# Performance work log

Hardware: AMD Instinct MI355X
Metric: run time of the kernel (lower is better)

The kernel has to match this reference:

```python
import math
import itertools
import jax, jax.numpy as jnp
import numpy as np

SEQ_LEN = 16
D_IN = 2048
TSS = 3          # temporal_set_size
D_OUT = 1128
PE_SCALE = 0.1
N_SUPPORT = 5
N_QUERIES = 1
LN_EPS = 1e-5


def _pos_enc(seq_len, d_model):
    pos = np.arange(seq_len, dtype=np.float32)[:, None]
    div = np.exp(np.arange(0, d_model, 2, dtype=np.float32) * -(math.log(10000.0) / d_model))
    pe = np.zeros((seq_len, d_model), dtype=np.float32)
    pe[:, 0::2] = np.sin(pos * div) * PE_SCALE
    pe[:, 1::2] = np.cos(pos * div) * PE_SCALE
    return jnp.asarray(pe)


def _tuples(seq_len, k):
    return np.asarray(list(itertools.combinations(range(seq_len), k)), dtype=np.int32)  # [T, k]


def setup_inputs() -> dict:
    key = jax.random.key(0)
    ks = jax.random.split(key, 8)
    return {
        "support_set": jax.random.normal(ks[0], (N_SUPPORT, SEQ_LEN, D_IN), jnp.float32),
        "queries": jax.random.normal(ks[1], (N_QUERIES, SEQ_LEN, D_IN), jnp.float32),
        "support_labels": jnp.arange(N_SUPPORT, dtype=jnp.int64),
        "wk": jax.random.normal(ks[2], (D_OUT, D_IN * TSS), jnp.float32) * 0.02,
        "bk": jax.random.normal(ks[3], (D_OUT,), jnp.float32) * 0.02,
        "wv": jax.random.normal(ks[4], (D_OUT, D_IN * TSS), jnp.float32) * 0.02,
        "bv": jax.random.normal(ks[5], (D_OUT,), jnp.float32) * 0.02,
        "gamma": jnp.ones((D_OUT,), jnp.float32),
        "beta": jnp.zeros((D_OUT,), jnp.float32),
    }


def _layer_norm(x, gamma, beta):
    mu = jnp.mean(x, axis=-1, keepdims=True)
    var = jnp.mean(jnp.square(x - mu), axis=-1, keepdims=True)
    return (x - mu) * jax.lax.rsqrt(var + LN_EPS) * gamma + beta


def reference(support_set, queries, support_labels, wk, bk, wv, bv, gamma, beta):
    tup = _tuples(SEQ_LEN, TSS)                      # [T, 3] static
    T = tup.shape[0]                                 # tuples_len = C(16,3) = 560
    pe = _pos_enc(SEQ_LEN, D_IN)                     # [S, D_IN]

    s = support_set + pe                             # [5, S, D_IN]
    q = queries + pe                                 # [1, S, D_IN]

    # gather frame tuples and flatten: [n, T, 3*D_IN]
    s_t = s[:, tup, :].reshape(N_SUPPORT, T, TSS * D_IN)
    q_t = q[:, tup, :].reshape(N_QUERIES, T, TSS * D_IN)

    s_ks = _layer_norm(s_t @ wk.T + bk, gamma, beta)  # [5, T, D_OUT]
    q_ks = _layer_norm(q_t @ wk.T + bk, gamma, beta)  # [1, T, D_OUT]
    s_vs = s_t @ wv.T + bv                            # [5, T, D_OUT]
    q_vs = q_t @ wv.T + bv                            # [1, T, D_OUT]

    # _extract_class_indices returns the label value itself -> direct row gather
    ck = s_ks[support_labels]                         # [C, T, D_OUT]
    cv = s_vs[support_labels]                         # [C, T, D_OUT]

    scores = jnp.einsum('qtd,csd->cqts', q_ks, ck) / math.sqrt(D_OUT)  # [C, Q, T, T]
    attn = jax.nn.softmax(scores, axis=-1)            # softmax over support tuples
    proto = jnp.einsum('cqts,csd->cqtd', attn, cv)    # [C, Q, T, D_OUT]

    diff = q_vs[None] - proto                         # [C, Q, T, D_OUT]
    dist = -jnp.sum(diff * diff, axis=(-2, -1)) / T   # [C, Q]
    logits = dist.T                                   # [Q, C]
    return logits
```

## Files before the change

kernel.cpp:

```cpp
#include <hip/hip_runtime.h>
#include <hip/hip_bf16.h>

#define SEQ 16
#define DIN 2048
#define TSS 3
#define DOUT 1128
#define DPAD 1152
#define NT 560
#define NTPAD 576
#define NSEQ 6
#define NCOL 6768

typedef __attribute__((ext_vector_type(4))) float f32x4;
typedef __attribute__((ext_vector_type(8))) short bf16x8;

__device__ __forceinline__ float bf2f(unsigned short h) {
    union { unsigned int u; float f; } c; c.u = ((unsigned int)h) << 16; return c.f;
}
__device__ __forceinline__ unsigned short f2bf(float f) {
    union { float f; unsigned int u; } c; c.f = f;
    unsigned int lsb = (c.u >> 16) & 1;
    c.u += 0x7fffu + lsb;
    return (unsigned short)(c.u >> 16);
}
__device__ __forceinline__ float loadf(const void* p, size_t i, int f32m) {
    return f32m ? ((const float*)p)[i] : bf2f(((const unsigned short*)p)[i]);
}
__device__ __forceinline__ void load8(const void* p, int o, int f32m, float* out) {
    if (f32m) {
        f32x4 x0 = *(const f32x4*)((const float*)p + o);
        f32x4 x1 = *(const f32x4*)((const float*)p + o + 4);
#pragma unroll
        for (int j = 0; j < 4; ++j) { out[j] = x0[j]; out[4 + j] = x1[j]; }
    } else {
        bf16x8 h = *(const bf16x8*)((const unsigned short*)p + o);
#pragma unroll
        for (int j = 0; j < 8; ++j) out[j] = bf2f((unsigned short)h[j]);
    }
}
__device__ __forceinline__ int probe_f32(const void* gamma) {
    return (((const unsigned int*)gamma)[0] == 0x3F800000u) ? 1 : 0;
}
__device__ __forceinline__ int probe_i64(const void* labels) {
    return (((const long long*)labels)[1] == 1LL) ? 1 : 0;
}
__device__ __forceinline__ int get_label(const void* p, int c, int is64) {
    long long v = is64 ? ((const long long*)p)[c] : (long long)((const int*)p)[c];
    if (v < 0) v = 0; if (v > 4) v = 4;
    return (int)v;
}


__global__ __launch_bounds__(256) void k_build_x(
        const void* __restrict__ sup, const void* __restrict__ qry,
        const void* __restrict__ gamma,
        unsigned short* __restrict__ XF) {
    int f32m = probe_f32(gamma);
    int c8 = blockIdx.x * 256 + threadIdx.x;
    int idx512 = c8 >> 6;
    int rowgrp = idx512 >> 6, kt = idx512 & 63;
    int sub = c8 & 63;
    int r15 = sub & 15;
    int row = rowgrp * 16 + r15;
    int f = row & 15, n = row >> 4;
    int k = kt * 32 + (sub >> 4) * 8;
    bf16x8 ov;
#pragma unroll
    for (int j = 0; j < 8; ++j) {
        int d = k + j;
        float v = (n < 5) ? loadf(sup, (size_t)row * DIN + d, f32m)
                          : loadf(qry, (size_t)f * DIN + d, f32m);
        int m2 = d & ~1;
        float div = __expf(-(float)m2 * (9.210340371976184f / 2048.0f));
        float ang = (float)f * div;
        float pe = ((d & 1) ? __cosf(ang) : __sinf(ang)) * 0.1f;
        ov[j] = (short)f2bf(v + pe);
    }
    *(bf16x8*)(XF + (size_t)c8 * 8) = ov;
}

__global__ __launch_bounds__(512) void k_proj(
        const unsigned short* __restrict__ XF,
        const void* __restrict__ wk, const void* __restrict__ wv,
        const void* __restrict__ gamma,
        unsigned short* __restrict__ Pb) {
    int f32m = probe_f32(gamma);
    int cg = blockIdx.x;
    int tid = threadIdx.x;
    int w = tid >> 6, lane = tid & 63;
    int c16 = lane & 15, quad = lane >> 4;
    int col = cg * 16 + c16;
    int which = col / 3384; int rem = col - which * 3384;
    int seg = rem / DOUT;   int o = rem - seg * DOUT;
    const void* src = which ? wv : wk;
    size_t sbase = (size_t)o * (TSS * DIN) + (size_t)seg * DIN + (size_t)quad * 8;
    const unsigned short* aF = XF + lane * 8;

    f32x4 acc[6];
#pragma unroll
    for (int m = 0; m < 6; ++m) acc[m] = (f32x4){0.f, 0.f, 0.f, 0.f};

    int ktb = w * 8;
    if (f32m) {
        const float* s32 = (const float*)src + sbase;
#pragma unroll 2
        for (int kt = ktb; kt < ktb + 8; ++kt) {
            f32x4 w0 = *(const f32x4*)(s32 + (size_t)kt * 32);
            f32x4 w1 = *(const f32x4*)(s32 + (size_t)kt * 32 + 4);
            bf16x8 b;
#pragma unroll
            for (int j = 0; j < 4; ++j) {
                b[j]     = (short)f2bf(w0[j]);
                b[4 + j] = (short)f2bf(w1[j]);
            }
#pragma unroll
            for (int m = 0; m < 6; ++m) {
                bf16x8 a = *(const bf16x8*)(aF + ((size_t)(m * 64 + kt) << 9));
                acc[m] = __builtin_amdgcn_mfma_f32_16x16x32_bf16(a, b, acc[m], 0, 0, 0);
            }
        }
    } else {
        const unsigned short* s16 = (const unsigned short*)src + sbase;
#pragma unroll 2
        for (int kt = ktb; kt < ktb + 8; ++kt) {
            bf16x8 b = *(const bf16x8*)(s16 + (size_t)kt * 32);
#pragma unroll
            for (int m = 0; m < 6; ++m) {
                bf16x8 a = *(const bf16x8*)(aF + ((size_t)(m * 64 + kt) << 9));
                acc[m] = __builtin_amdgcn_mfma_f32_16x16x32_bf16(a, b, acc[m], 0, 0, 0);
            }
        }
    }

    __shared__ float red[8 * 6 * 64 * 4];
#pragma unroll
    for (int m = 0; m < 6; ++m)
#pragma unroll
        for (int r = 0; r < 4; ++r)
            red[(((w) * 6 + m) * 64 + lane) * 4 + r] = acc[m][r];
    __syncthreads();
    if (w < 6) {
        int m = w;
#pragma unroll
        for (int r = 0; r < 4; ++r) {
            float s = 0.f;
#pragma unroll
            for (int k = 0; k < 8; ++k)
                s += red[((k * 6 + m) * 64 + lane) * 4 + r];
            int row = m * 16 + quad * 4 + r;
            Pb[(size_t)row * NCOL + col] = f2bf(s);
        }
    }
}

__global__ __launch_bounds__(192) void k_combine_ln(
        const unsigned short* __restrict__ Pb,
        const void* __restrict__ bk, const void* __restrict__ bv,
        const void* __restrict__ gamma, const void* __restrict__ beta,
        unsigned short* __restrict__ ksF, unsigned short* __restrict__ vs) {
    int n = blockIdx.x / NT, t = blockIdx.x % NT;
    int f32m = probe_f32(gamma);
    int idx = t, fi, fj, fk;
    for (fi = 0;; ++fi) { int c2 = (15 - fi) * (14 - fi) / 2; if (idx < c2) break; idx -= c2; }
    for (fj = fi + 1;; ++fj) { int c1 = 15 - fj; if (idx < c1) break; idx -= c1; }
    fk = fj + 1 + idx;
    size_t ri = (size_t)(n * 16 + fi) * NCOL;
    size_t rj = (size_t)(n * 16 + fj) * NCOL;
    size_t rk = (size_t)(n * 16 + fk) * NCOL;

    int c = threadIdx.x;
    int o = c * 8;
    float av[8], bvv[8];
    float s = 0.f, s2 = 0.f;
    if (c < 141) {
        bf16x8 p0 = *(const bf16x8*)(Pb + ri + o);
        bf16x8 p1 = *(const bf16x8*)(Pb + rj + DOUT + o);
        bf16x8 p2 = *(const bf16x8*)(Pb + rk + 2 * DOUT + o);
        bf16x8 p3 = *(const bf16x8*)(Pb + ri + 3 * DOUT + o);
        bf16x8 p4 = *(const bf16x8*)(Pb + rj + 4 * DOUT + o);
        bf16x8 p5 = *(const bf16x8*)(Pb + rk + 5 * DOUT + o);
        float kb[8], vb[8];
        load8(bk, o, f32m, kb);
        load8(bv, o, f32m, vb);
#pragma unroll
        for (int e = 0; e < 8; ++e) {
            float a = bf2f((unsigned short)p0[e]) + bf2f((unsigned short)p1[e])
                    + bf2f((unsigned short)p2[e]) + kb[e];
            float b = bf2f((unsigned short)p3[e]) + bf2f((unsigned short)p4[e])
                    + bf2f((unsigned short)p5[e]) + vb[e];
            av[e] = a; bvv[e] = b;
            s += a; s2 += a * a;
        }
    }
    __shared__ float red[6];
#pragma unroll
    for (int off = 32; off; off >>= 1) { s += __shfl_down(s, off); s2 += __shfl_down(s2, off); }
    int wid = threadIdx.x >> 6;
    if ((threadIdx.x & 63) == 0) { red[wid] = s; red[3 + wid] = s2; }
    __syncthreads();
    s = red[0] + red[1] + red[2];
    s2 = red[3] + red[4] + red[5];
    float mu = s / (float)DOUT;
    float var = s2 / (float)DOUT - mu * mu;
    float rstd = rsqrtf(var + 1e-5f);

    size_t ntbase = ((size_t)(n * 36 + (t >> 4)) * 36) * 512 + (size_t)(t & 15) * 8;
    size_t vbase = ((size_t)n * NT + t) * DPAD;
    if (c < 144) {
        bf16x8 kout = (bf16x8){0, 0, 0, 0, 0, 0, 0, 0};
        bf16x8 vout = (bf16x8){0, 0, 0, 0, 0, 0, 0, 0};
        if (c < 141) {
            float gb[8], be[8];
            load8(gamma, o, f32m, gb);
            load8(beta, o, f32m, be);
#pragma unroll
            for (int e = 0; e < 8; ++e) {
                kout[e] = (short)f2bf((av[e] - mu) * rstd * gb[e] + be[e]);
                vout[e] = (short)f2bf(bvv[e]);
            }
        }
        *(bf16x8*)(ksF + ntbase + ((size_t)(c >> 2) << 9) + ((size_t)(c & 3) << 7)) = kout;
        *(bf16x8*)(vs + vbase + o) = vout;
    }
}

__global__ __launch_bounds__(128) void k_transpose(
        const unsigned short* __restrict__ vs, unsigned short* __restrict__ vsTF) {
    int b = blockIdx.x;
    int tt = b % 18; b /= 18; int ot = b % 36; int n = b / 36;
    int t0 = tt * 32, o0 = ot * 32;
    int tid = threadIdx.x;
    __shared__ unsigned short tile[32][33];
    {
        int tl = tid >> 2, ch = tid & 3;
        int t = t0 + tl;
        bf16x8 v = (bf16x8){0, 0, 0, 0, 0, 0, 0, 0};
        if (t < NT) v = *(const bf16x8*)(vs + ((size_t)n * NT + t) * DPAD + o0 + ch * 8);
#pragma unroll
        for (int j = 0; j < 8; ++j) tile[tl][ch * 8 + j] = (unsigned short)v[j];
    }
    __syncthreads();
    {
        int r = tid >> 2, g = tid & 3;
        union { unsigned short u[8]; bf16x8 v; } pk;
#pragma unroll
        for (int e = 0; e < 8; ++e) pk.u[e] = tile[g * 8 + e][r];
        size_t addr = ((size_t)(n * 72 + ot * 2 + (r >> 4)) * 18 + tt) * 512
                    + (size_t)(g * 16 + (r & 15)) * 8;
        *(bf16x8*)(vsTF + addr) = pk.v;
    }
}

__global__ __launch_bounds__(256) void k_scores(
        const unsigned short* __restrict__ ksF, const void* __restrict__ labels,
        float* __restrict__ scores) {
    int b = blockIdx.x;
    int c = b % 5; int rest = b / 5;
    int tm = rest / 9, tn = rest % 9;
    int tid = threadIdx.x;
    int w = tid >> 6, lane = tid & 63;
    int c16 = lane & 15, quad = lane >> 4;
    int lab = get_label(labels, c, probe_i64(labels));
    const unsigned short* aF[4];
    const unsigned short* bF[4];
#pragma unroll
    for (int i = 0; i < 4; ++i) {
        aF[i] = ksF + (((size_t)(5 * 36 + tm * 4 + i) * 36) << 9) + lane * 8;
        bF[i] = ksF + (((size_t)(lab * 36 + tn * 4 + i) * 36) << 9) + lane * 8;
    }
    f32x4 acc[4][4];
#pragma unroll
    for (int i = 0; i < 4; ++i)
#pragma unroll
        for (int j = 0; j < 4; ++j) acc[i][j] = (f32x4){0.f, 0.f, 0.f, 0.f};

    int ktb = w * 9;
#pragma unroll 2
    for (int kt = ktb; kt < ktb + 9; ++kt) {
        bf16x8 a[4], bv4[4];
#pragma unroll
        for (int i = 0; i < 4; ++i) a[i]   = *(const bf16x8*)(aF[i] + ((size_t)kt << 9));
#pragma unroll
        for (int j = 0; j < 4; ++j) bv4[j] = *(const bf16x8*)(bF[j] + ((size_t)kt << 9));
#pragma unroll
        for (int i = 0; i < 4; ++i)
#pragma unroll
            for (int j = 0; j < 4; ++j)
                acc[i][j] = __builtin_amdgcn_mfma_f32_16x16x32_bf16(a[i], bv4[j], acc[i][j], 0, 0, 0);
    }
    __shared__ float red[16 * 3 * 64 * 4];
#pragma unroll
    for (int i = 0; i < 4; ++i) {
        if (i != w) {
            int slot = (w < i) ? w : w - 1;
#pragma unroll
            for (int j = 0; j < 4; ++j)
#pragma unroll
                for (int r = 0; r < 4; ++r)
                    red[(((i * 4 + j) * 3 + slot) * 64 + lane) * 4 + r] = acc[i][j][r];
        }
    }
    __syncthreads();
    {
        const float scale = 0.029774540f;
        f32x4 own[4];
        if (w == 0)      { own[0]=acc[0][0]; own[1]=acc[0][1]; own[2]=acc[0][2]; own[3]=acc[0][3]; }
        else if (w == 1) { own[0]=acc[1][0]; own[1]=acc[1][1]; own[2]=acc[1][2]; own[3]=acc[1][3]; }
        else if (w == 2) { own[0]=acc[2][0]; own[1]=acc[2][1]; own[2]=acc[2][2]; own[3]=acc[2][3]; }
        else             { own[0]=acc[3][0]; own[1]=acc[3][1]; own[2]=acc[3][2]; own[3]=acc[3][3]; }
#pragma unroll
        for (int j = 0; j < 4; ++j) {
            int t = w * 4 + j;
#pragma unroll
            for (int r = 0; r < 4; ++r) {
                float s = 0.f;
#pragma unroll
                for (int k = 0; k < 4; ++k) {
                    if (k == w) s += own[j][r];
                    else {
                        int slot = k - (k > w ? 1 : 0);
                        s += red[((t * 3 + slot) * 64 + lane) * 4 + r];
                    }
                }
                int tq = tm * 64 + w * 16 + quad * 4 + r;
                int ts = tn * 64 + j * 16 + c16;
                scores[((size_t)c * NTPAD + tq) * NTPAD + ts] = s * scale;
            }
        }
    }
}

__global__ __launch_bounds__(256) void k_softmax(
        const float* __restrict__ scores, unsigned short* __restrict__ attnF) {
    int row = blockIdx.x * 4 + (threadIdx.x >> 6);
    int lane = threadIdx.x & 63;
    int c = row / NTPAD, tq = row % NTPAD;
    unsigned short* dstc = attnF + ((size_t)(c * 36 + (tq >> 4)) * 18) * 512 + (size_t)(tq & 15) * 8;
    if (tq >= NT) {
#pragma unroll
        for (int i = 0; i < 9; ++i) {
            int ts = lane + i * 64;
            dstc[((ts >> 5) << 9) + ((ts >> 3) & 3) * 128 + (ts & 7)] = 0;
        }
        return;
    }
    const float* src = scores + (size_t)row * NTPAD;
    float vals[9];
    float m = -1e30f;
#pragma unroll
    for (int i = 0; i < 9; ++i) {
        int idx = lane + i * 64;
        vals[i] = (idx < NT) ? src[idx] : -1e30f;
        m = fmaxf(m, vals[i]);
    }
#pragma unroll
    for (int off = 32; off; off >>= 1) m = fmaxf(m, __shfl_xor(m, off));
    float s = 0.f;
#pragma unroll
    for (int i = 0; i < 9; ++i) {
        int idx = lane + i * 64;
        vals[i] = (idx < NT) ? __expf(vals[i] - m) : 0.f;
        s += vals[i];
    }
#pragma unroll
    for (int off = 32; off; off >>= 1) s += __shfl_xor(s, off);
    float inv = 1.f / s;
#pragma unroll
    for (int i = 0; i < 9; ++i) {
        int ts = lane + i * 64;
        dstc[((ts >> 5) << 9) + ((ts >> 3) & 3) * 128 + (ts & 7)] =
            (ts < NT) ? f2bf(vals[i] * inv) : 0;
    }
}

__global__ __launch_bounds__(128) void k_proto_dist(
        const unsigned short* __restrict__ attnF, const unsigned short* __restrict__ vs,
        const unsigned short* __restrict__ vsTF,
        const void* __restrict__ labels, float* __restrict__ parts) {
    int b = blockIdx.x;
    int c = b / 162; int rest = b % 162;
    int tm = rest / 18, tn = rest % 18;
    int tid = threadIdx.x;
    int w = tid >> 6, lane = tid & 63;
    int c16 = lane & 15, quad = lane >> 4;
    int lab = get_label(labels, c, probe_i64(labels));
    const unsigned short* aF = attnF + ((size_t)(c * 36 + tm * 4) * 18) * 512 + lane * 8;
    const unsigned short* bF = vsTF + ((size_t)(lab * 72 + tn * 4) * 18) * 512 + lane * 8;
    f32x4 acc[4][4];
#pragma unroll
    for (int i = 0; i < 4; ++i)
#pragma unroll
        for (int j = 0; j < 4; ++j) acc[i][j] = (f32x4){0.f, 0.f, 0.f, 0.f};

    int ktb = w * 9;
#pragma unroll 2
    for (int kt = ktb; kt < ktb + 9; ++kt) {
        bf16x8 a[4], bv4[4];
#pragma unroll
        for (int i = 0; i < 4; ++i) a[i]   = *(const bf16x8*)(aF + ((size_t)(i * 18 + kt) << 9));
#pragma unroll
        for (int j = 0; j < 4; ++j) bv4[j] = *(const bf16x8*)(bF + ((size_t)(j * 18 + kt) << 9));
#pragma unroll
        for (int i = 0; i < 4; ++i)
#pragma unroll
            for (int j = 0; j < 4; ++j)
                acc[i][j] = __builtin_amdgcn_mfma_f32_16x16x32_bf16(a[i], bv4[j], acc[i][j], 0, 0, 0);
    }
    __shared__ float red[16 * 64 * 4];
    if (w == 0) {
#pragma unroll
        for (int i = 2; i < 4; ++i)
#pragma unroll
            for (int j = 0; j < 4; ++j)
#pragma unroll
                for (int r = 0; r < 4; ++r)
                    red[((i * 4 + j) * 64 + lane) * 4 + r] = acc[i][j][r];
    } else {
#pragma unroll
        for (int i = 0; i < 2; ++i)
#pragma unroll
            for (int j = 0; j < 4; ++j)
#pragma unroll
                for (int r = 0; r < 4; ++r)
                    red[((i * 4 + j) * 64 + lane) * 4 + r] = acc[i][j][r];
    }
    __syncthreads();
    {
        const unsigned short* qv = vs + (size_t)5 * NT * DPAD;
        float part = 0.f;
        if (w == 0) {
#pragma unroll
            for (int i = 0; i < 2; ++i)
#pragma unroll
                for (int j = 0; j < 4; ++j)
#pragma unroll
                    for (int r = 0; r < 4; ++r) {
                        float s = acc[i][j][r] + red[((i * 4 + j) * 64 + lane) * 4 + r];
                        int tq = tm * 64 + i * 16 + quad * 4 + r;
                        int o  = tn * 64 + j * 16 + c16;
                        if (tq < NT && o < DOUT) {
                            float d = bf2f(qv[(size_t)tq * DPAD + o]) - s;
                            part += d * d;
                        }
                    }
        } else {
#pragma unroll
            for (int i = 2; i < 4; ++i)
#pragma unroll
                for (int j = 0; j < 4; ++j)
#pragma unroll
                    for (int r = 0; r < 4; ++r) {
                        float s = acc[i][j][r] + red[((i * 4 + j) * 64 + lane) * 4 + r];
                        int tq = tm * 64 + i * 16 + quad * 4 + r;
                        int o  = tn * 64 + j * 16 + c16;
                        if (tq < NT && o < DOUT) {
                            float d = bf2f(qv[(size_t)tq * DPAD + o]) - s;
                            part += d * d;
                        }
                    }
        }
#pragma unroll
        for (int off = 32; off; off >>= 1) part += __shfl_down(part, off);
        if (lane == 0) parts[blockIdx.x * 2 + w] = part;
    }
}

__global__ __launch_bounds__(320) void k_final(const float* __restrict__ parts,
                                               const void* __restrict__ gamma,
                                               void* __restrict__ out) {
    int c = threadIdx.x >> 6;
    int lane = threadIdx.x & 63;
    float s = 0.f;
    for (int i = lane; i < 324; i += 64) s += parts[c * 324 + i];
#pragma unroll
    for (int off = 32; off; off >>= 1) s += __shfl_down(s, off);
    if (lane == 0) {
        float v = -s * (1.0f / (float)NT);
        if (probe_f32(gamma)) ((float*)out)[c] = v;
        else ((unsigned short*)out)[c] = f2bf(v);
    }
}

extern "C" void kernel_launch(void* const* d_in, const int* in_sizes, int n_in,
                              void* d_out, int out_size, void* d_ws, size_t ws_size,
                              hipStream_t stream) {
    const void* sup   = d_in[0];
    const void* qry   = d_in[1];
    const void* labs  = d_in[2];
    const void* wk    = d_in[3];
    const void* bk    = d_in[4];
    const void* wv    = d_in[5];
    const void* bv    = d_in[6];
    const void* gamma = d_in[7];
    const void* beta  = d_in[8];

    char* ws = (char*)d_ws;
    unsigned short* XF     = (unsigned short*)(ws + 256);
    unsigned short* Pb     = (unsigned short*)(ws + 393472);
    float*          parts  = (float*)(ws + 2992384);
    unsigned short* ksF    = (unsigned short*)(ws + 33326080);
    unsigned short* vsb    = (unsigned short*)(ws + 41288704);
    float*          scores = (float*)(ws + 49030144);
    unsigned short* attnF  = (unsigned short*)(ws + 55665664);
    unsigned short* vsTF   = (unsigned short*)(ws + 58983424);

    k_build_x   <<<96, 256, 0, stream>>>(sup, qry, gamma, XF);
    k_proj      <<<423, 512, 0, stream>>>(XF, wk, wv, gamma, Pb);
    k_combine_ln<<<NSEQ * NT, 192, 0, stream>>>(Pb, bk, bv, gamma, beta, ksF, vsb);
    k_transpose <<<5 * 36 * 18, 128, 0, stream>>>(vsb, vsTF);
    k_scores    <<<405, 256, 0, stream>>>(ksF, labs, scores);
    k_softmax   <<<720, 256, 0, stream>>>(scores, attnF);
    k_proto_dist<<<810, 128, 0, stream>>>(attnF, vsb, vsTF, labs, parts);
    k_final     <<<1, 320, 0, stream>>>(parts, gamma, d_out);
}
```

Baseline: 176.4 us.

## Merge transpose into scores kernel and fold final reduction via last-block atomic

```diff
diff --git a/kernel.cpp b/kernel.cpp
--- a/kernel.cpp
+++ b/kernel.cpp
@@ -157,7 +157,9 @@
         const unsigned short* __restrict__ Pb,
         const void* __restrict__ bk, const void* __restrict__ bv,
         const void* __restrict__ gamma, const void* __restrict__ beta,
-        unsigned short* __restrict__ ksF, unsigned short* __restrict__ vs) {
+        unsigned short* __restrict__ ksF, unsigned short* __restrict__ vs,
+        unsigned int* __restrict__ counter) {
+    if (blockIdx.x == 0 && threadIdx.x == 0) *counter = 0;
     int n = blockIdx.x / NT, t = blockIdx.x % NT;
     int f32m = probe_f32(gamma);
     int idx = t, fi, fj, fk;
@@ -224,108 +226,109 @@
     }
 }
 
-__global__ __launch_bounds__(128) void k_transpose(
-        const unsigned short* __restrict__ vs, unsigned short* __restrict__ vsTF) {
-    int b = blockIdx.x;
-    int tt = b % 18; b /= 18; int ot = b % 36; int n = b / 36;
-    int t0 = tt * 32, o0 = ot * 32;
-    int tid = threadIdx.x;
-    __shared__ unsigned short tile[32][33];
-    {
-        int tl = tid >> 2, ch = tid & 3;
-        int t = t0 + tl;
-        bf16x8 v = (bf16x8){0, 0, 0, 0, 0, 0, 0, 0};
-        if (t < NT) v = *(const bf16x8*)(vs + ((size_t)n * NT + t) * DPAD + o0 + ch * 8);
-#pragma unroll
-        for (int j = 0; j < 8; ++j) tile[tl][ch * 8 + j] = (unsigned short)v[j];
-    }
-    __syncthreads();
-    {
-        int r = tid >> 2, g = tid & 3;
-        union { unsigned short u[8]; bf16x8 v; } pk;
-#pragma unroll
-        for (int e = 0; e < 8; ++e) pk.u[e] = tile[g * 8 + e][r];
-        size_t addr = ((size_t)(n * 72 + ot * 2 + (r >> 4)) * 18 + tt) * 512
-                    + (size_t)(g * 16 + (r & 15)) * 8;
-        *(bf16x8*)(vsTF + addr) = pk.v;
-    }
-}
-
-__global__ __launch_bounds__(256) void k_scores(
-        const unsigned short* __restrict__ ksF, const void* __restrict__ labels,
-        float* __restrict__ scores) {
-    int b = blockIdx.x;
-    int c = b % 5; int rest = b / 5;
-    int tm = rest / 9, tn = rest % 9;
-    int tid = threadIdx.x;
-    int w = tid >> 6, lane = tid & 63;
-    int c16 = lane & 15, quad = lane >> 4;
-    int lab = get_label(labels, c, probe_i64(labels));
-    const unsigned short* aF[4];
-    const unsigned short* bF[4];
-#pragma unroll
-    for (int i = 0; i < 4; ++i) {
-        aF[i] = ksF + (((size_t)(5 * 36 + tm * 4 + i) * 36) << 9) + lane * 8;
-        bF[i] = ksF + (((size_t)(lab * 36 + tn * 4 + i) * 36) << 9) + lane * 8;
-    }
-    f32x4 acc[4][4];
-#pragma unroll
-    for (int i = 0; i < 4; ++i)
-#pragma unroll
-        for (int j = 0; j < 4; ++j) acc[i][j] = (f32x4){0.f, 0.f, 0.f, 0.f};
-
-    int ktb = w * 9;
+__global__ __launch_bounds__(256) void k_scores_tr(
+        const unsigned short* __restrict__ ksF,
+        const unsigned short* __restrict__ vs, unsigned short* __restrict__ vsTF,
+        const void* __restrict__ labels, float* __restrict__ scores) {
+    __shared__ float red[16 * 3 * 64 * 4];
+    if (blockIdx.x < 405) {
+        int b = blockIdx.x;
+        int c = b % 5; int rest = b / 5;
+        int tm = rest / 9, tn = rest % 9;
+        int tid = threadIdx.x;
+        int w = tid >> 6, lane = tid & 63;
+        int c16 = lane & 15, quad = lane >> 4;
+        int lab = get_label(labels, c, probe_i64(labels));
+        const unsigned short* aF[4];
+        const unsigned short* bF[4];
+#pragma unroll
+        for (int i = 0; i < 4; ++i) {
+            aF[i] = ksF + (((size_t)(5 * 36 + tm * 4 + i) * 36) << 9) + lane * 8;
+            bF[i] = ksF + (((size_t)(lab * 36 + tn * 4 + i) * 36) << 9) + lane * 8;
+        }
+        f32x4 acc[4][4];
+#pragma unroll
+        for (int i = 0; i < 4; ++i)
+#pragma unroll
+            for (int j = 0; j < 4; ++j) acc[i][j] = (f32x4){0.f, 0.f, 0.f, 0.f};
+
+        int ktb = w * 9;
 #pragma unroll 2
-    for (int kt = ktb; kt < ktb + 9; ++kt) {
-        bf16x8 a[4], bv4[4];
-#pragma unroll
-        for (int i = 0; i < 4; ++i) a[i]   = *(const bf16x8*)(aF[i] + ((size_t)kt << 9));
-#pragma unroll
-        for (int j = 0; j < 4; ++j) bv4[j] = *(const bf16x8*)(bF[j] + ((size_t)kt << 9));
-#pragma unroll
-        for (int i = 0; i < 4; ++i)
-#pragma unroll
-            for (int j = 0; j < 4; ++j)
-                acc[i][j] = __builtin_amdgcn_mfma_f32_16x16x32_bf16(a[i], bv4[j], acc[i][j], 0, 0, 0);
-    }
-    __shared__ float red[16 * 3 * 64 * 4];
-#pragma unroll
-    for (int i = 0; i < 4; ++i) {
-        if (i != w) {
-            int slot = (w < i) ? w : w - 1;
-#pragma unroll
-            for (int j = 0; j < 4; ++j)
-#pragma unroll
-                for (int r = 0; r < 4; ++r)
-                    red[(((i * 4 + j) * 3 + slot) * 64 + lane) * 4 + r] = acc[i][j][r];
-        }
-    }
-    __syncthreads();
-    {
-        const float scale = 0.029774540f;
-        f32x4 own[4];
-        if (w == 0)      { own[0]=acc[0][0]; own[1]=acc[0][1]; own[2]=acc[0][2]; own[3]=acc[0][3]; }
-        else if (w == 1) { own[0]=acc[1][0]; own[1]=acc[1][1]; own[2]=acc[1][2]; own[3]=acc[1][3]; }
-        else if (w == 2) { own[0]=acc[2][0]; own[1]=acc[2][1]; own[2]=acc[2][2]; own[3]=acc[2][3]; }
-        else             { own[0]=acc[3][0]; own[1]=acc[3][1]; own[2]=acc[3][2]; own[3]=acc[3][3]; }
-#pragma unroll
-        for (int j = 0; j < 4; ++j) {
-            int t = w * 4 + j;
-#pragma unroll
-            for (int r = 0; r < 4; ++r) {
-                float s = 0.f;
-#pragma unroll
-                for (int k = 0; k < 4; ++k) {
-                    if (k == w) s += own[j][r];
-                    else {
-                        int slot = k - (k > w ? 1 : 0);
-                        s += red[((t * 3 + slot) * 64 + lane) * 4 + r];
+        for (int kt = ktb; kt < ktb + 9; ++kt) {
+            bf16x8 a[4], bv4[4];
+#pragma unroll
+            for (int i = 0; i < 4; ++i) a[i]   = *(const bf16x8*)(aF[i] + ((size_t)kt << 9));
+#pragma unroll
+            for (int j = 0; j < 4; ++j) bv4[j] = *(const bf16x8*)(bF[j] + ((size_t)kt << 9));
+#pragma unroll
+            for (int i = 0; i < 4; ++i)
+#pragma unroll
+                for (int j = 0; j < 4; ++j)
+                    acc[i][j] = __builtin_amdgcn_mfma_f32_16x16x32_bf16(a[i], bv4[j], acc[i][j], 0, 0, 0);
+        }
+#pragma unroll
+        for (int i = 0; i < 4; ++i) {
+            if (i != w) {
+                int slot = (w < i) ? w : w - 1;
+#pragma unroll
+                for (int j = 0; j < 4; ++j)
+#pragma unroll
+                    for (int r = 0; r < 4; ++r)
+                        red[(((i * 4 + j) * 3 + slot) * 64 + lane) * 4 + r] = acc[i][j][r];
+            }
+        }
+        __syncthreads();
+        {
+            const float scale = 0.029774540f;
+            f32x4 own[4];
+            if (w == 0)      { own[0]=acc[0][0]; own[1]=acc[0][1]; own[2]=acc[0][2]; own[3]=acc[0][3]; }
+            else if (w == 1) { own[0]=acc[1][0]; own[1]=acc[1][1]; own[2]=acc[1][2]; own[3]=acc[1][3]; }
+            else if (w == 2) { own[0]=acc[2][0]; own[1]=acc[2][1]; own[2]=acc[2][2]; own[3]=acc[2][3]; }
+            else             { own[0]=acc[3][0]; own[1]=acc[3][1]; own[2]=acc[3][2]; own[3]=acc[3][3]; }
+#pragma unroll
+            for (int j = 0; j < 4; ++j) {
+                int t = w * 4 + j;
+#pragma unroll
+                for (int r = 0; r < 4; ++r) {
+                    float s = 0.f;
+#pragma unroll
+                    for (int k = 0; k < 4; ++k) {
+                        if (k == w) s += own[j][r];
+                        else {
+                            int slot = k - (k > w ? 1 : 0);
+                            s += red[((t * 3 + slot) * 64 + lane) * 4 + r];
+                        }
                     }
+                    int tq = tm * 64 + w * 16 + quad * 4 + r;
+                    int ts = tn * 64 + j * 16 + c16;
+                    scores[((size_t)c * NTPAD + tq) * NTPAD + ts] = s * scale;
                 }
-                int tq = tm * 64 + w * 16 + quad * 4 + r;
-                int ts = tn * 64 + j * 16 + c16;
-                scores[((size_t)c * NTPAD + tq) * NTPAD + ts] = s * scale;
-            }
+            }
+        }
+    } else {
+        unsigned short (*tile2)[32][33] = (unsigned short (*)[32][33])red;
+        int b2 = blockIdx.x - 405;
+        int half = threadIdx.x >> 7, ltid = threadIdx.x & 127;
+        int tb = b2 * 2 + half;
+        int tt = tb % 18; tb /= 18; int ot = tb % 36; int n = tb / 36;
+        int t0 = tt * 32, o0 = ot * 32;
+        {
+            int tl = ltid >> 2, ch = ltid & 3;
+            int t = t0 + tl;
+            bf16x8 v = (bf16x8){0, 0, 0, 0, 0, 0, 0, 0};
+            if (t < NT) v = *(const bf16x8*)(vs + ((size_t)n * NT + t) * DPAD + o0 + ch * 8);
+#pragma unroll
+            for (int j = 0; j < 8; ++j) tile2[half][tl][ch * 8 + j] = (unsigned short)v[j];
+        }
+        __syncthreads();
+        {
+            int r = ltid >> 2, g = ltid & 3;
+            union { unsigned short u[8]; bf16x8 v; } pk;
+#pragma unroll
+            for (int e = 0; e < 8; ++e) pk.u[e] = tile2[half][g * 8 + e][r];
+            size_t addr = ((size_t)(n * 72 + ot * 2 + (r >> 4)) * 18 + tt) * 512
+                        + (size_t)(g * 16 + (r & 15)) * 8;
+            *(bf16x8*)(vsTF + addr) = pk.v;
         }
     }
 }
@@ -376,7 +379,9 @@
 __global__ __launch_bounds__(128) void k_proto_dist(
         const unsigned short* __restrict__ attnF, const unsigned short* __restrict__ vs,
         const unsigned short* __restrict__ vsTF,
-        const void* __restrict__ labels, float* __restrict__ parts) {
+        const void* __restrict__ labels, float* __restrict__ parts,
+        unsigned int* __restrict__ counter,
+        const void* __restrict__ gamma, void* __restrict__ out) {
     int b = blockIdx.x;
     int c = b / 162; int rest = b % 162;
     int tm = rest / 18, tn = rest % 18;
@@ -463,21 +468,25 @@
         for (int off = 32; off; off >>= 1) part += __shfl_down(part, off);
         if (lane == 0) parts[blockIdx.x * 2 + w] = part;
     }
-}
-
-__global__ __launch_bounds__(320) void k_final(const float* __restrict__ parts,
-                                               const void* __restrict__ gamma,
-                                               void* __restrict__ out) {
-    int c = threadIdx.x >> 6;
-    int lane = threadIdx.x & 63;
-    float s = 0.f;
-    for (int i = lane; i < 324; i += 64) s += parts[c * 324 + i];
-#pragma unroll
-    for (int off = 32; off; off >>= 1) s += __shfl_down(s, off);
-    if (lane == 0) {
-        float v = -s * (1.0f / (float)NT);
-        if (probe_f32(gamma)) ((float*)out)[c] = v;
-        else ((unsigned short*)out)[c] = f2bf(v);
+    __syncthreads();
+    __threadfence();
+    __shared__ unsigned int lastflag;
+    if (tid == 0) lastflag = atomicAdd(counter, 1);
+    __syncthreads();
+    if (lastflag == 809) {
+        __threadfence();
+        const volatile float* pv = parts;
+        for (int cc = w; cc < 5; cc += 2) {
+            float s = 0.f;
+            for (int i = lane; i < 324; i += 64) s += pv[cc * 324 + i];
+#pragma unroll
+            for (int off = 32; off; off >>= 1) s += __shfl_down(s, off);
+            if (lane == 0) {
+                float v = -s * (1.0f / (float)NT);
+                if (probe_f32(gamma)) ((float*)out)[cc] = v;
+                else ((unsigned short*)out)[cc] = f2bf(v);
+            }
+        }
     }
 }
 
@@ -498,6 +507,7 @@
     unsigned short* XF     = (unsigned short*)(ws + 256);
     unsigned short* Pb     = (unsigned short*)(ws + 393472);
     float*          parts  = (float*)(ws + 2992384);
+    unsigned int*   counter= (unsigned int*)(ws + 3002368);
     unsigned short* ksF    = (unsigned short*)(ws + 33326080);
     unsigned short* vsb    = (unsigned short*)(ws + 41288704);
     float*          scores = (float*)(ws + 49030144);
@@ -506,10 +516,8 @@
 
     k_build_x   <<<96, 256, 0, stream>>>(sup, qry, gamma, XF);
     k_proj      <<<423, 512, 0, stream>>>(XF, wk, wv, gamma, Pb);
-    k_combine_ln<<<NSEQ * NT, 192, 0, stream>>>(Pb, bk, bv, gamma, beta, ksF, vsb);
-    k_transpose <<<5 * 36 * 18, 128, 0, stream>>>(vsb, vsTF);
-    k_scores    <<<405, 256, 0, stream>>>(ksF, labs, scores);
+    k_combine_ln<<<NSEQ * NT, 192, 0, stream>>>(Pb, bk, bv, gamma, beta, ksF, vsb, counter);
+    k_scores_tr <<<405 + 1620, 256, 0, stream>>>(ksF, vsb, vsTF, labs, scores);
     k_softmax   <<<720, 256, 0, stream>>>(scores, attnF);
-    k_proto_dist<<<810, 128, 0, stream>>>(attnF, vsb, vsTF, labs, parts);
-    k_final     <<<1, 320, 0, stream>>>(parts, gamma, d_out);
-}
+    k_proto_dist<<<810, 128, 0, stream>>>(attnF, vsb, vsTF, labs, parts, counter, gamma, d_out);
+}
```

After: 197.4 us. 1.12x slower.
